# Kernel optimization log

Hardware: AMD Instinct MI355X
Metric: run time of the kernel (lower is better)

The kernel has to match this reference:

```python
import jax, jax.numpy as jnp
import numpy as np

N = 12000   # nodes (multiple of 120)
E = 192000  # edges
T = 120     # utterances per dialogue
IN = 192
OUT = 6


def _edge_softmax(logits, dst, n):
    # logits: [E, H] -> softmax over incoming edges of each dst node
    m = jax.ops.segment_max(logits, dst, num_segments=n)
    ex = jnp.exp(logits - m[dst])
    s = jax.ops.segment_sum(ex, dst, num_segments=n)
    return ex / s[dst]


def _gatv2(h, src, dst, Wsrc, bsrc, Wdst, bdst, attn, Wres, n):
    # DGL GATv2Conv: e = attn . leakyrelu(fc_src(h)[u] + fc_dst(h)[v]), residual, relu activation
    Hh, F = attn.shape
    fs = (h @ Wsrc + bsrc).reshape(n, Hh, F)
    fd = (h @ Wdst + bdst).reshape(n, Hh, F)
    e = jax.nn.leaky_relu(fs[src] + fd[dst], 0.2)          # [E, H, F]
    logits = jnp.einsum('ehf,hf->eh', e, attn)              # [E, H]
    alpha = _edge_softmax(logits, dst, n)                   # [E, H]
    out = jax.ops.segment_sum(alpha[:, :, None] * fs[src], dst, num_segments=n)
    res = (h @ Wres).reshape(n, Hh, F)
    return jax.nn.relu(out + res)                           # [N, H, F]


def _lstm_dir(x, Wih, Whh, bih, bhh, reverse):
    # x: [T, B, D]; torch gate order i, f, g, o
    B = x.shape[1]
    hid = Whh.shape[1]
    def step(carry, xt):
        h, c = carry
        z = xt @ Wih.T + h @ Whh.T + bih + bhh
        i, f, g, o = jnp.split(z, 4, axis=-1)
        c = jax.nn.sigmoid(f) * c + jax.nn.sigmoid(i) * jnp.tanh(g)
        h = jax.nn.sigmoid(o) * jnp.tanh(c)
        return (h, c), h
    init = (jnp.zeros((B, hid), x.dtype), jnp.zeros((B, hid), x.dtype))
    _, hs = jax.lax.scan(step, init, x, reverse=reverse)
    return hs


def setup_inputs() -> dict:
    key = jax.random.key(0)
    ks = iter(jax.random.split(key, 64))
    def rn(shape, s=0.05):
        return jax.random.normal(next(ks), shape, jnp.float32) * s
    inp = {
        'text': rn((N, 1024), 1.0),
        'audio': rn((N, 512), 1.0),
        'vision': rn((N, 1024), 1.0),
        'edge_src': jax.random.randint(next(ks), (E,), 0, N, jnp.int32),
        'edge_dst': jax.random.randint(next(ks), (E,), 0, N, jnp.int32),
        # modality encoders
        'W_audio': rn((512, 64)), 'b_audio': jnp.zeros((64,), jnp.float32),
        'W_vision': rn((1024, 64)), 'b_vision': jnp.zeros((64,), jnp.float32),
        'W_text': rn((1024, 64)), 'b_text': jnp.zeros((64,), jnp.float32),
        # bidirectional LSTM (hidden=4 -> 16 gate rows)
        'Wih_f': rn((16, IN)), 'Whh_f': rn((16, 4)), 'bih_f': jnp.zeros((16,), jnp.float32), 'bhh_f': jnp.zeros((16,), jnp.float32),
        'Wih_b': rn((16, IN)), 'Whh_b': rn((16, 4)), 'bih_b': jnp.zeros((16,), jnp.float32), 'bhh_b': jnp.zeros((16,), jnp.float32),
        # imputation GraphConv (192->192, norm='both')
        'W_gc': rn((IN, IN)), 'b_gc': jnp.zeros((IN,), jnp.float32),
        # gat2 (cross-modal multi-head GAT, 192 -> 16 heads x 4)
        'Wsrc2': rn((IN, 64)), 'bsrc2': jnp.zeros((64,), jnp.float32),
        'Wdst2': rn((IN, 64)), 'bdst2': jnp.zeros((64,), jnp.float32),
        'attn2': rn((16, 4)), 'Wres2': rn((IN, 64)),
        # gat1 layer 0 (192 -> 16 heads x 32)
        'Wsrc0': rn((IN, 512)), 'bsrc0': jnp.zeros((512,), jnp.float32),
        'Wdst0': rn((IN, 512)), 'bdst0': jnp.zeros((512,), jnp.float32),
        'attn0': rn((16, 32)), 'Wres0': rn((IN, 512)),
        # gat1 layer 1 (512 -> 16 heads x 4)
        'Wsrc1': rn((512, 64)), 'bsrc1': jnp.zeros((64,), jnp.float32),
        'Wdst1': rn((512, 64)), 'bdst1': jnp.zeros((64,), jnp.float32),
        'attn1': rn((16, 4)), 'Wres1': rn((512, 64)),
        # final classifier Linear(136, out_size)
        'W_lin': rn((136, OUT)), 'b_lin': jnp.zeros((OUT,), jnp.float32),
    }
    return inp


def reference(text, audio, vision, edge_src, edge_dst,
              W_audio, b_audio, W_vision, b_vision, W_text, b_text,
              Wih_f, Whh_f, bih_f, bhh_f, Wih_b, Whh_b, bih_b, bhh_b,
              W_gc, b_gc,
              Wsrc2, bsrc2, Wdst2, bdst2, attn2, Wres2,
              Wsrc0, bsrc0, Wdst0, bdst0, attn0, Wres0,
              Wsrc1, bsrc1, Wdst1, bdst1, attn1, Wres1,
              W_lin, b_lin):
    n = text.shape[0]
    # modality encoders (dropout is identity at inference)
    t = text @ W_text + b_text
    a = audio @ W_audio + b_audio
    v = vision @ W_vision + b_vision
    stackFT = jnp.concatenate([t, a, v], axis=1)            # [N, 192]

    # bidirectional LSTM over dialogues of length T=120
    x = stackFT.reshape(-1, T, IN).transpose(1, 0, 2)       # [T, B, 192]
    hf = _lstm_dir(x, Wih_f, Whh_f, bih_f, bhh_f, False)
    hb = _lstm_dir(x, Wih_b, Whh_b, bih_b, bhh_b, True)
    newFeature = jnp.concatenate([hf, hb], -1).transpose(1, 0, 2).reshape(n, 8)

    # GraphConv imputation, norm='both' (degrees clamped to 1 as in DGL)
    ones = jnp.ones((edge_src.shape[0],), stackFT.dtype)
    deg_out = jnp.maximum(jax.ops.segment_sum(ones, edge_src, num_segments=n), 1.0)
    deg_in = jnp.maximum(jax.ops.segment_sum(ones, edge_dst, num_segments=n), 1.0)
    hw = (stackFT @ W_gc) * (deg_out ** -0.5)[:, None]
    h1 = jax.ops.segment_sum(hw[edge_src], edge_dst, num_segments=n) * (deg_in ** -0.5)[:, None] + b_gc
    h = 0.5 * (stackFT + h1)
    # F.normalize(h, p=1)
    h = h / jnp.maximum(jnp.sum(jnp.abs(h), axis=1, keepdims=True), 1e-12)

    # cross-modal multi-head GAT branch -> [N, 64]
    h3 = _gatv2(h, edge_src, edge_dst, Wsrc2, bsrc2, Wdst2, bdst2, attn2, Wres2, n).reshape(n, -1)

    # stacked GATv2 layers
    h = _gatv2(h, edge_src, edge_dst, Wsrc0, bsrc0, Wdst0, bdst0, attn0, Wres0, n).reshape(n, -1)  # [N, 512]
    h = _gatv2(h, edge_src, edge_dst, Wsrc1, bsrc1, Wdst1, bdst1, attn1, Wres1, n).reshape(n, -1)  # [N, 64]

    out = jnp.concatenate([h, newFeature, h3], axis=1) @ W_lin + b_lin  # [N, out_size]
    return out
```

## Files before the change

### kernel.cpp

```cpp
#include <hip/hip_runtime.h>

typedef __attribute__((ext_vector_type(8))) short short8;
typedef __attribute__((ext_vector_type(4))) float f32x4;
typedef _Float16 half8v __attribute__((ext_vector_type(8)));
typedef _Float16 half4v __attribute__((ext_vector_type(4)));

__device__ __forceinline__ unsigned short f2bf(float f) {
    unsigned u = __float_as_uint(f);
    u += 0x7FFFu + ((u >> 16) & 1u);
    return (unsigned short)(u >> 16);
}
__device__ __forceinline__ float bf2f(unsigned short h) {
    return __uint_as_float((unsigned)h << 16);
}

template<int MF, int OUTMODE>
__global__ __launch_bounds__(256)
void gemm_v7(const unsigned short* __restrict__ A, const unsigned short* __restrict__ B,
             const float* __restrict__ bias, const float* __restrict__ rowscale,
             void* __restrict__ Cv, const float* __restrict__ fin_num,
             const float* __restrict__ fin_den,
             int M, int Nb, int K, int ldc)
{
    __shared__ alignas(16) unsigned short As[MF * 64 * 32];
    __shared__ alignas(16) unsigned short Bs[4 * 64 * 8];
    const int t = threadIdx.x;
    const int w = t >> 6, l = t & 63;
    const int r16 = l & 15, kg = l >> 4;
    const int row0 = blockIdx.x * (64 * MF);
    const int col0 = blockIdx.y * 64;
    const int bcol = t & 63, bkg = t >> 6;

    f32x4 acc[MF][4] = {};
    const short8 z8 = {0, 0, 0, 0, 0, 0, 0, 0};

    int srow[MF], sch[MF];
    bool va[MF];
    const unsigned short* aptr[MF];
#pragma unroll
    for (int it = 0; it < MF; ++it) {
        int idx = it * 256 + t;
        srow[it] = idx >> 2; sch[it] = idx & 3;
        int gm = row0 + srow[it];
        va[it] = gm < M;
        aptr[it] = A + (size_t)gm * K + sch[it] * 8;
    }
    const unsigned short* bptr = B + (size_t)(bkg * 8) * Nb + col0 + bcol;

    short8 pa[MF];
    unsigned short pbv[8];
#pragma unroll
    for (int it = 0; it < MF; ++it)
        pa[it] = va[it] ? *reinterpret_cast<const short8*>(aptr[it]) : z8;
#pragma unroll
    for (int j = 0; j < 8; ++j) pbv[j] = bptr[(size_t)j * Nb];

    for (int k0 = 0; k0 < K; k0 += 32) {
#pragma unroll
        for (int it = 0; it < MF; ++it)
            *reinterpret_cast<short8*>(&As[srow[it] * 32 + sch[it] * 8]) = pa[it];
        {
            short8 hv;
#pragma unroll
            for (int j = 0; j < 8; ++j) hv[j] = (short)pbv[j];
            *reinterpret_cast<short8*>(&Bs[bkg * 512 + bcol * 8]) = hv;
        }
        __syncthreads();
        if (k0 + 32 < K) {
#pragma unroll
            for (int it = 0; it < MF; ++it)
                pa[it] = va[it] ? *reinterpret_cast<const short8*>(aptr[it] + k0 + 32) : z8;
#pragma unroll
            for (int j = 0; j < 8; ++j) pbv[j] = bptr[(size_t)(k0 + 32 + j) * Nb];
        }
        short8 af[MF];
#pragma unroll
        for (int mi = 0; mi < MF; ++mi)
            af[mi] = *reinterpret_cast<const short8*>(&As[((w * MF + mi) * 16 + r16) * 32 + kg * 8]);
#pragma unroll
        for (int ni = 0; ni < 4; ++ni) {
            short8 bf = *reinterpret_cast<const short8*>(&Bs[kg * 512 + (ni * 16 + r16) * 8]);
#pragma unroll
            for (int mi = 0; mi < MF; ++mi)
                acc[mi][ni] = __builtin_amdgcn_mfma_f32_16x16x32_bf16(af[mi], bf, acc[mi][ni], 0, 0, 0);
        }
        __syncthreads();
    }
#pragma unroll
    for (int mi = 0; mi < MF; ++mi)
#pragma unroll
        for (int ni = 0; ni < 4; ++ni) {
            int col = col0 + ni * 16 + r16;
            float bv = bias ? bias[col] : 0.f;
#pragma unroll
            for (int r = 0; r < 4; ++r) {
                int gm = row0 + (w * MF + mi) * 16 + kg * 4 + r;
                if (gm < M) {
                    float val = acc[mi][ni][r] + bv;
                    if (rowscale) val *= rowscale[gm];
                    size_t idx = (size_t)gm * ldc + col;
                    if (OUTMODE == 0) {
                        ((float*)Cv)[idx] = val;
                    } else if (OUTMODE == 1) {
                        ((unsigned short*)Cv)[idx] = f2bf(val);
                    } else {
                        float d = fin_den[(size_t)gm * 16 + (col >> 5)];
                        float inv = (d > 0.f) ? __fdividef(1.f, d) : 0.f;
                        float o = fmaxf(fin_num[idx] * inv + val, 0.f);
                        ((unsigned short*)Cv)[idx] = f2bf(o);
                    }
                }
            }
        }
}

__global__ __launch_bounds__(256)
void enc_f16(const float* __restrict__ text, const float* __restrict__ audio, const float* __restrict__ vision,
             const _Float16* __restrict__ Wf16,
             const float* __restrict__ bt, const float* __restrict__ ba, const float* __restrict__ bv,
             float* __restrict__ Cf, unsigned short* __restrict__ Cb, int M)
{
    __shared__ alignas(16) _Float16 Af[32 * 32];
    __shared__ alignas(16) _Float16 Bf[4 * 64 * 8];
    const int z = blockIdx.z;
    const float* A  = (z == 0) ? text : (z == 1) ? audio : vision;
    const _Float16* W = Wf16 + ((z == 0) ? 0 : (z == 1) ? 65536 : 98304);
    const float* bb = (z == 0) ? bt : (z == 1) ? ba : bv;
    const int K = (z == 1) ? 512 : 1024;

    const int t = threadIdx.x;
    const int w = t >> 6, l = t & 63;
    const int r16 = l & 15, kg = l >> 4;
    const int row0 = blockIdx.x * 32;
    const int mi = w & 1;
    const int ncol0 = (w >> 1) * 32;
    const int arow = t >> 3, ac8 = t & 7;
    const int bcol = t & 63, bkg = t >> 6;

    const float* ap = A + (size_t)(row0 + arow) * K + ac8 * 4;
    const _Float16* wp = W + (size_t)(bkg * 8) * 64 + bcol;

    float4 pa = *reinterpret_cast<const float4*>(ap);
    _Float16 pb[8];
#pragma unroll
    for (int j = 0; j < 8; ++j) pb[j] = wp[(size_t)j * 64];

    f32x4 acc[2] = {};
    for (int k0 = 0; k0 < K; k0 += 32) {
        {
            half4v av;
            av[0] = (_Float16)pa.x; av[1] = (_Float16)pa.y;
            av[2] = (_Float16)pa.z; av[3] = (_Float16)pa.w;
            *reinterpret_cast<half4v*>(&Af[arow * 32 + ac8 * 4]) = av;
            half8v bv8;
#pragma unroll
            for (int j = 0; j < 8; ++j) bv8[j] = pb[j];
            *reinterpret_cast<half8v*>(&Bf[bkg * 512 + bcol * 8]) = bv8;
        }
        __syncthreads();
        if (k0 + 32 < K) {
            pa = *reinterpret_cast<const float4*>(ap + k0 + 32);
#pragma unroll
            for (int j = 0; j < 8; ++j) pb[j] = wp[(size_t)(k0 + 32 + j) * 64];
        }
        half8v af = *reinterpret_cast<const half8v*>(&Af[(mi * 16 + r16) * 32 + kg * 8]);
#pragma unroll
        for (int ni = 0; ni < 2; ++ni) {
            half8v bf = *reinterpret_cast<const half8v*>(&Bf[kg * 512 + (ncol0 + ni * 16 + r16) * 8]);
            acc[ni] = __builtin_amdgcn_mfma_f32_16x16x32_f16(af, bf, acc[ni], 0, 0, 0);
        }
        __syncthreads();
    }
#pragma unroll
    for (int ni = 0; ni < 2; ++ni) {
        int col = ncol0 + ni * 16 + r16;
        float bvv = bb[col];
#pragma unroll
        for (int r = 0; r < 4; ++r) {
            int gr = row0 + mi * 16 + kg * 4 + r;
            if (gr < M) {
                float val = acc[ni][r] + bvv;
                size_t idx = (size_t)gr * 192 + z * 64 + col;
                Cf[idx] = val;
                Cb[idx] = f2bf(val);
            }
        }
    }
}

__global__ void pack3b(const float* __restrict__ W0, const float* __restrict__ W1, const float* __restrict__ W2,
                       const float* __restrict__ b0, const float* __restrict__ b1,
                       unsigned short* __restrict__ Wp, float* __restrict__ bp, int K, int O)
{
    int gid = blockIdx.x * blockDim.x + threadIdx.x;
    int O3 = 3 * O;
    if (gid < O3) bp[gid] = (gid < O) ? b0[gid] : (gid < 2 * O) ? b1[gid - O] : 0.f;
    if (gid >= K * O3) return;
    int k = gid / O3, c = gid - k * O3;
    float v = (c < O) ? W0[k * O + c] : (c < 2 * O) ? W1[k * O + c - O] : W2[k * O + c - 2 * O];
    Wp[gid] = f2bf(v);
}

__global__ void pack2b(const float* __restrict__ W0, const float* __restrict__ W1,
                       const float* __restrict__ b0, const float* __restrict__ b1,
                       unsigned short* __restrict__ Wp, float* __restrict__ bp, int K, int O)
{
    int gid = blockIdx.x * blockDim.x + threadIdx.x;
    int O2 = 2 * O;
    if (gid < O2) bp[gid] = (gid < O) ? b0[gid] : b1[gid - O];
    if (gid >= K * O2) return;
    int k = gid / O2, c = gid - k * O2;
    Wp[gid] = f2bf((c < O) ? W0[k * O + c] : W1[k * O + c - O]);
}

__global__ void pack1b(const float* __restrict__ W, unsigned short* __restrict__ Wp, int cnt)
{
    int gid = blockIdx.x * blockDim.x + threadIdx.x;
    if (gid < cnt) Wp[gid] = f2bf(W[gid]);
}

__global__ void pack_encw(const float* __restrict__ Wt, const float* __restrict__ Wa, const float* __restrict__ Wv,
                          _Float16* __restrict__ out)
{
    int gid = blockIdx.x * blockDim.x + threadIdx.x;
    if (gid >= 163840) return;
    float v;
    if (gid < 65536) v = Wt[gid];
    else if (gid < 98304) v = Wa[gid - 65536];
    else v = Wv[gid - 98304];
    out[gid] = (_Float16)v;
}

__global__ void deg_kernel(const int* __restrict__ src, const int* __restrict__ dst,
                           int* degout, int* degin, int E)
{
    int e = blockIdx.x * blockDim.x + threadIdx.x;
    if (e < E) {
        atomicAdd(&degout[src[e]], 1);
        atomicAdd(&degin[dst[e]], 1);
    }
}

__global__ __launch_bounds__(1024)
void scan_kernel(const int* __restrict__ degin, int* __restrict__ rowstart, int n)
{
    __shared__ int part[1024];
    int t = threadIdx.x;
    int chunk = (n + 1023) / 1024;
    int s = 0;
    for (int i = 0; i < chunk; ++i) {
        int idx = t * chunk + i;
        if (idx < n) s += degin[idx];
    }
    part[t] = s;
    __syncthreads();
    for (int o = 1; o < 1024; o <<= 1) {
        int v = (t >= o) ? part[t - o] : 0;
        __syncthreads();
        part[t] += v;
        __syncthreads();
    }
    int run = (t > 0) ? part[t - 1] : 0;
    for (int i = 0; i < chunk; ++i) {
        int idx = t * chunk + i;
        if (idx < n) { rowstart[idx] = run; run += degin[idx]; }
    }
    if (t == 1023) rowstart[n] = part[1023];
}

__global__ void perm_kernel(const int* __restrict__ dst, const int* __restrict__ rowstart,
                            int* cursor, int* __restrict__ perm, int E)
{
    int e = blockIdx.x * blockDim.x + threadIdx.x;
    if (e < E) {
        int v = dst[e];
        int p = atomicAdd(&cursor[v], 1);
        perm[rowstart[v] + p] = e;
    }
}

__global__ void gather_src_kernel(const int* __restrict__ esrc, int* perm, int E)
{
    int i = blockIdx.x * blockDim.x + threadIdx.x;
    if (i < E) perm[i] = esrc[perm[i]];
}

__global__ void rs_kernel(const int* degout, const int* degin, float* rso, float* rsi, int n)
{
    int i = blockIdx.x * blockDim.x + threadIdx.x;
    if (i < n) {
        rso[i] = rsqrtf((float)max(degout[i], 1));
        rsi[i] = rsqrtf((float)max(degin[i], 1));
    }
}

__global__ void lstm_pre(const float* __restrict__ x, const float* __restrict__ Wf,
                         const float* __restrict__ Wb,
                         const float* bf1, const float* bf2, const float* bb1, const float* bb2,
                         float* __restrict__ xWf, float* __restrict__ xWb, int n)
{
    int gid = blockIdx.x * blockDim.x + threadIdx.x;
    if (gid >= n * 32) return;
    int nn = gid >> 5, r = gid & 31, d = r >> 4, j = r & 15;
    const float* W = (d ? Wb : Wf) + j * 192;
    const float* xr = x + (size_t)nn * 192;
    float s = 0.f;
#pragma unroll 4
    for (int k = 0; k < 192; k += 4) {
        float4 xv = *reinterpret_cast<const float4*>(xr + k);
        float4 wv = *reinterpret_cast<const float4*>(W + k);
        s += xv.x * wv.x + xv.y * wv.y + xv.z * wv.z + xv.w * wv.w;
    }
    s += d ? (bb1[j] + bb2[j]) : (bf1[j] + bf2[j]);
    int b = nn / 120, tt = nn - b * 120;
    (d ? xWb : xWf)[((size_t)b * 16 + j) * 120 + tt] = s;
}

__device__ __forceinline__ float fsigm(float x) { return __fdividef(1.f, 1.f + __expf(-x)); }
__device__ __forceinline__ float ftanh(float x) { return 1.f - __fdividef(2.f, __expf(2.f * x) + 1.f); }

template<int DIR>
__device__ void lstm_chain(const float* __restrict__ xw, const float* __restrict__ whh,
                           float* __restrict__ newF, int b)
{
    int j = threadIdx.x & 15;
    int k = j & 3;
    float4 w = *reinterpret_cast<const float4*>(whh + j * 4);
    const float* xp = xw + ((size_t)b * 16 + j) * 120;
    float h0 = 0.f, h1 = 0.f, h2 = 0.f, h3 = 0.f, cst = 0.f;
    int tb0 = DIR ? 108 : 0;
    float4 a0 = *reinterpret_cast<const float4*>(xp + tb0);
    float4 a1 = *reinterpret_cast<const float4*>(xp + tb0 + 4);
    float4 a2 = *reinterpret_cast<const float4*>(xp + tb0 + 8);
    for (int ch = 0; ch < 10; ++ch) {
        float4 b0 = a0, b1 = a1, b2 = a2;
        if (ch < 9) {
            int nt = DIR ? (96 - ch * 12) : (12 + ch * 12);
            b0 = *reinterpret_cast<const float4*>(xp + nt);
            b1 = *reinterpret_cast<const float4*>(xp + nt + 4);
            b2 = *reinterpret_cast<const float4*>(xp + nt + 8);
        }
        float zz[12] = {a0.x, a0.y, a0.z, a0.w, a1.x, a1.y, a1.z, a1.w, a2.x, a2.y, a2.z, a2.w};
        int tbase = DIR ? (108 - ch * 12) : (ch * 12);
#pragma unroll
        for (int ii = 0; ii < 12; ++ii) {
            int idx = DIR ? (11 - ii) : ii;
            float z = zz[idx] + ((w.x * h0 + w.y * h1) + (w.z * h2 + w.w * h3));
            float zi = __shfl(z, k, 16);
            float zf = __shfl(z, k + 4, 16);
            float zg = __shfl(z, k + 8, 16);
            float zo = __shfl(z, k + 12, 16);
            float ig = fsigm(zi), fg = fsigm(zf), gg = ftanh(zg), og = fsigm(zo);
            cst = fg * cst + ig * gg;
            float hn = og * ftanh(cst);
            h0 = __shfl(hn, 0, 16); h1 = __shfl(hn, 1, 16);
            h2 = __shfl(hn, 2, 16); h3 = __shfl(hn, 3, 16);
            if (j < 4) newF[((size_t)b * 120 + tbase + idx) * 8 + DIR * 4 + j] = hn;
        }
        a0 = b0; a1 = b1; a2 = b2;
    }
}

__global__ __launch_bounds__(64)
void lstm_seq2(const float* __restrict__ xWf, const float* __restrict__ xWb,
               const float* __restrict__ Whhf, const float* __restrict__ Whhb,
               float* __restrict__ newF, int B)
{
    int sub = threadIdx.x >> 4;
    int chain = blockIdx.x * 4 + sub;
    if (chain >= 2 * B) return;
    int d = chain / B;
    int b = chain - d * B;
    if (d == 0) lstm_chain<0>(xWf, Whhf, newF, b);
    else        lstm_chain<1>(xWb, Whhb, newF, b);
}

__global__ __launch_bounds__(256)
void gc_combine5(const float* __restrict__ stackFT, const unsigned short* __restrict__ hw,
                 const int* __restrict__ rowstart, const int* __restrict__ csrc,
                 const float* __restrict__ rs_in,
                 const float* __restrict__ b_gc, unsigned short* __restrict__ hB, int n)
{
    int v = blockIdx.x * 4 + (threadIdx.x >> 6);
    int l = threadIdx.x & 63;
    if (v >= n) return;
    int s0 = rowstart[v], s1 = rowstart[v + 1];
    float sum0 = 0.f, sum1 = 0.f, sum2 = 0.f;

    unsigned short a0 = 0, a1 = 0, a2 = 0, b0 = 0, b1 = 0, b2 = 0;
    auto LD = [&](int i, unsigned short& x0, unsigned short& x1, unsigned short& x2) {
        const unsigned short* hr = hw + (size_t)csrc[i] * 192 + l;
        x0 = hr[0]; x1 = hr[64]; x2 = hr[128];
    };
    int i = s0;
    if (i < s1) LD(i, a0, a1, a2);
    if (i + 1 < s1) LD(i + 1, b0, b1, b2);
    for (; i + 2 < s1; i += 2) {
        unsigned short n0, n1, n2, m0 = 0, m1 = 0, m2 = 0;
        LD(i + 2, n0, n1, n2);
        if (i + 3 < s1) LD(i + 3, m0, m1, m2);
        sum0 += bf2f(a0) + bf2f(b0);
        sum1 += bf2f(a1) + bf2f(b1);
        sum2 += bf2f(a2) + bf2f(b2);
        a0 = n0; a1 = n1; a2 = n2; b0 = m0; b1 = m1; b2 = m2;
    }
    if (i < s1) { sum0 += bf2f(a0); sum1 += bf2f(a1); sum2 += bf2f(a2); }
    if (i + 1 < s1) { sum0 += bf2f(b0); sum1 += bf2f(b1); sum2 += bf2f(b2); }

    float ri = rs_in[v];
    const float* sf = stackFT + (size_t)v * 192 + l;
    float v0 = 0.5f * (sf[0]   + sum0 * ri + b_gc[l]);
    float v1 = 0.5f * (sf[64]  + sum1 * ri + b_gc[l + 64]);
    float v2 = 0.5f * (sf[128] + sum2 * ri + b_gc[l + 128]);
    float r = fabsf(v0) + fabsf(v1) + fabsf(v2);
#pragma unroll
    for (int o = 32; o; o >>= 1) r += __shfl_xor(r, o);
    float inv = __fdividef(1.f, fmaxf(r, 1e-12f));
    unsigned short* hp = hB + (size_t)v * 192 + l;
    hp[0]   = f2bf(v0 * inv);
    hp[64]  = f2bf(v1 * inv);
    hp[128] = f2bf(v2 * inv);
}

__global__ __launch_bounds__(256)
void gat_edge4c(const unsigned short* __restrict__ base,
                const float* __restrict__ attn,
                const int* __restrict__ rowstart, const int* __restrict__ csrc,
                float* __restrict__ outp, int n)
{
    int v = blockIdx.x * 16 + (threadIdx.x >> 4);
    int l = threadIdx.x & 15;
    if (v >= n) return;
    float4 at = *reinterpret_cast<const float4*>(attn + l * 4);
    ushort4 fdu = *reinterpret_cast<const ushort4*>(base + (size_t)v * 192 + 64 + l * 4);
    float fd0 = bf2f(fdu.x), fd1 = bf2f(fdu.y), fd2 = bf2f(fdu.z), fd3 = bf2f(fdu.w);
    float ac0 = 0.f, ac1 = 0.f, ac2 = 0.f, ac3 = 0.f, dn = 0.f;
    int s0 = rowstart[v], s1 = rowstart[v + 1];

    auto LD = [&](int i) -> ushort4 {
        return *reinterpret_cast<const ushort4*>(base + (size_t)csrc[i] * 192 + l * 4);
    };
    auto ACC = [&](ushort4 su) {
        float s0f = bf2f(su.x), s1f = bf2f(su.y), s2f = bf2f(su.z), s3f = bf2f(su.w);
        float e0 = s0f + fd0; e0 = fmaxf(e0, 0.2f * e0);
        float e1 = s1f + fd1; e1 = fmaxf(e1, 0.2f * e1);
        float e2 = s2f + fd2; e2 = fmaxf(e2, 0.2f * e2);
        float e3 = s3f + fd3; e3 = fmaxf(e3, 0.2f * e3);
        float p = e0 * at.x + e1 * at.y + e2 * at.z + e3 * at.w;
        float ex = __expf(p);
        ac0 += ex * s0f; ac1 += ex * s1f; ac2 += ex * s2f; ac3 += ex * s3f;
        dn += ex;
    };
    const ushort4 zu = make_ushort4(0, 0, 0, 0);
    ushort4 c0 = zu, c1 = zu;
    int i = s0;
    if (i < s1) c0 = LD(i);
    if (i + 1 < s1) c1 = LD(i + 1);
    for (; i + 2 < s1; i += 2) {
        ushort4 n0 = LD(i + 2);
        ushort4 n1 = (i + 3 < s1) ? LD(i + 3) : zu;
        ACC(c0); ACC(c1);
        c0 = n0; c1 = n1;
    }
    if (i < s1) ACC(c0);
    if (i + 1 < s1) ACC(c1);

    ushort4 ru = *reinterpret_cast<const ushort4*>(base + (size_t)v * 192 + 128 + l * 4);
    float inv = (dn > 0.f) ? __fdividef(1.f, dn) : 0.f;
    float4 o;
    o.x = fmaxf(ac0 * inv + bf2f(ru.x), 0.f);
    o.y = fmaxf(ac1 * inv + bf2f(ru.y), 0.f);
    o.z = fmaxf(ac2 * inv + bf2f(ru.z), 0.f);
    o.w = fmaxf(ac3 * inv + bf2f(ru.w), 0.f);
    *reinterpret_cast<float4*>(outp + (size_t)v * 64 + l * 4) = o;
}

__global__ __launch_bounds__(256)
void gat_edge32b(const unsigned short* __restrict__ base,
                 const float* __restrict__ attn,
                 const int* __restrict__ rowstart, const int* __restrict__ csrc,
                 float* __restrict__ num, float* __restrict__ den, int n)
{
    int v = blockIdx.x * 4 + (threadIdx.x >> 6);
    int l = threadIdx.x & 63;
    if (v >= n) return;
    float at[8];
    {
        float4 aA = *reinterpret_cast<const float4*>(attn + l * 8);
        float4 aB = *reinterpret_cast<const float4*>(attn + l * 8 + 4);
        at[0] = aA.x; at[1] = aA.y; at[2] = aA.z; at[3] = aA.w;
        at[4] = aB.x; at[5] = aB.y; at[6] = aB.z; at[7] = aB.w;
    }
    float fd[8];
    {
        short8 fdu = *reinterpret_cast<const short8*>(base + (size_t)v * 1024 + 512 + l * 8);
#pragma unroll
        for (int j = 0; j < 8; ++j) fd[j] = bf2f((unsigned short)fdu[j]);
    }
    float acc[8] = {};
    float dn = 0.f;
    int s0 = rowstart[v], s1 = rowstart[v + 1];

    auto LD = [&](int i) -> short8 {
        return *reinterpret_cast<const short8*>(base + (size_t)csrc[i] * 1024 + l * 8);
    };
    auto ACC = [&](short8 su) {
        float sf[8];
        float p = 0.f;
#pragma unroll
        for (int j = 0; j < 8; ++j) {
            sf[j] = bf2f((unsigned short)su[j]);
            float e = sf[j] + fd[j];
            e = fmaxf(e, 0.2f * e);
            p += e * at[j];
        }
        p += __shfl_xor(p, 1, 4);
        p += __shfl_xor(p, 2, 4);
        float ex = __expf(p);
#pragma unroll
        for (int j = 0; j < 8; ++j) acc[j] += ex * sf[j];
        dn += ex;
    };
    const short8 z8 = {0, 0, 0, 0, 0, 0, 0, 0};
    short8 c0 = z8, c1 = z8;
    int i = s0;
    if (i < s1) c0 = LD(i);
    if (i + 1 < s1) c1 = LD(i + 1);
    for (; i + 2 < s1; i += 2) {
        short8 n0 = LD(i + 2);
        short8 n1 = (i + 3 < s1) ? LD(i + 3) : z8;
        ACC(c0); ACC(c1);
        c0 = n0; c1 = n1;
    }
    if (i < s1) ACC(c0);
    if (i + 1 < s1) ACC(c1);

    float* np = num + (size_t)v * 512 + l * 8;
    *reinterpret_cast<float4*>(np)     = make_float4(acc[0], acc[1], acc[2], acc[3]);
    *reinterpret_cast<float4*>(np + 4) = make_float4(acc[4], acc[5], acc[6], acc[7]);
    if ((l & 3) == 0) den[(size_t)v * 16 + (l >> 2)] = dn;
}

__global__ void final_lin(const float* __restrict__ h1, const float* __restrict__ newF,
                          const float* __restrict__ h3, const float* __restrict__ W,
                          const float* __restrict__ bias, float* __restrict__ out, int n)
{
    int gid = blockIdx.x * blockDim.x + threadIdx.x;
    if (gid >= n * 6) return;
    int v = gid / 6, o = gid - v * 6;
    float s = bias[o];
    const float* a = h1 + (size_t)v * 64;
#pragma unroll 8
    for (int r = 0; r < 64; ++r) s += a[r] * W[r * 6 + o];
    const float* b = newF + (size_t)v * 8;
#pragma unroll
    for (int r = 0; r < 8; ++r) s += b[r] * W[(64 + r) * 6 + o];
    const float* c = h3 + (size_t)v * 64;
#pragma unroll 8
    for (int r = 0; r < 64; ++r) s += c[r] * W[(72 + r) * 6 + o];
    out[gid] = s;
}

extern "C" void kernel_launch(void* const* d_in, const int* in_sizes, int n_in,
                              void* d_out, int out_size, void* d_ws, size_t ws_size,
                              hipStream_t stream)
{
    const float* text   = (const float*)d_in[0];
    const float* audio  = (const float*)d_in[1];
    const float* vision = (const float*)d_in[2];
    const int*   esrc   = (const int*)d_in[3];
    const int*   edst   = (const int*)d_in[4];
    const float* W_audio = (const float*)d_in[5];  const float* b_audio = (const float*)d_in[6];
    const float* W_vision= (const float*)d_in[7];  const float* b_vision= (const float*)d_in[8];
    const float* W_text  = (const float*)d_in[9];  const float* b_text  = (const float*)d_in[10];
    const float* Wih_f = (const float*)d_in[11]; const float* Whh_f = (const float*)d_in[12];
    const float* bih_f = (const float*)d_in[13]; const float* bhh_f = (const float*)d_in[14];
    const float* Wih_b = (const float*)d_in[15]; const float* Whh_b = (const float*)d_in[16];
    const float* bih_b = (const float*)d_in[17]; const float* bhh_b = (const float*)d_in[18];
    const float* W_gc  = (const float*)d_in[19]; const float* b_gc  = (const float*)d_in[20];
    const float* Wsrc2 = (const float*)d_in[21]; const float* bsrc2 = (const float*)d_in[22];
    const float* Wdst2 = (const float*)d_in[23]; const float* bdst2 = (const float*)d_in[24];
    const float* attn2 = (const float*)d_in[25]; const float* Wres2 = (const float*)d_in[26];
    const float* Wsrc0 = (const float*)d_in[27]; const float* bsrc0 = (const float*)d_in[28];
    const float* Wdst0 = (const float*)d_in[29]; const float* bdst0 = (const float*)d_in[30];
    const float* attn0 = (const float*)d_in[31]; const float* Wres0 = (const float*)d_in[32];
    const float* Wsrc1 = (const float*)d_in[33]; const float* bsrc1 = (const float*)d_in[34];
    const float* Wdst1 = (const float*)d_in[35]; const float* bdst1 = (const float*)d_in[36];
    const float* attn1 = (const float*)d_in[37]; const float* Wres1 = (const float*)d_in[38];
    const float* W_lin = (const float*)d_in[39]; const float* b_lin = (const float*)d_in[40];
    float* out = (float*)d_out;

    const int n = in_sizes[0] / 1024;
    const int E = in_sizes[3];
    const int B = n / 120;

    char* p = (char*)d_ws;
    auto alloc_f = [&](size_t cnt) { float* r = (float*)p; p += ((cnt * 4 + 255) / 256) * 256; return r; };
    auto alloc_h = [&](size_t cnt) { unsigned short* r = (unsigned short*)p; p += ((cnt * 2 + 255) / 256) * 256; return r; };
    auto alloc_i = [&](size_t cnt) { int* r = (int*)p; p += ((cnt * 4 + 255) / 256) * 256; return r; };
    float*          stackFT = alloc_f((size_t)n * 192);
    unsigned short* stackBF = alloc_h((size_t)n * 192);
    unsigned short* hbufBF  = alloc_h((size_t)n * 192);
    unsigned short* encW    = alloc_h(163840);
    float* xWf     = alloc_f((size_t)n * 16);
    float* xWb     = alloc_f((size_t)n * 16);
    float* newF    = alloc_f((size_t)n * 8);
    float* big0    = alloc_f((size_t)n * 512);
    float* big1    = alloc_f((size_t)n * 512);
    float* big2    = alloc_f((size_t)n * 512);
    float* den     = alloc_f((size_t)n * 16);
    float* h3      = alloc_f((size_t)n * 64);
    float* h1s     = alloc_f((size_t)n * 64);
    float* rs_out  = alloc_f(n);
    float* rs_in   = alloc_f(n);
    int* zero_base = alloc_i((size_t)3 * n);
    int* degout = zero_base;
    int* degin  = zero_base + n;
    int* cursor = zero_base + 2 * n;
    int* rowstart = alloc_i((size_t)n + 1);
    int* perm     = alloc_i((size_t)E);
    if ((size_t)(p - (char*)d_ws) > ws_size) return;

    unsigned short* pw = (unsigned short*)h1s;
    float* pb = h1s + 120000;

    hipMemsetAsync(zero_base, 0, (size_t)3 * n * 4, stream);
    deg_kernel<<<(E + 255) / 256, 256, 0, stream>>>(esrc, edst, degout, degin, E);
    scan_kernel<<<1, 1024, 0, stream>>>(degin, rowstart, n);
    perm_kernel<<<(E + 255) / 256, 256, 0, stream>>>(edst, rowstart, cursor, perm, E);
    gather_src_kernel<<<(E + 255) / 256, 256, 0, stream>>>(esrc, perm, E);
    rs_kernel<<<(n + 255) / 256, 256, 0, stream>>>(degout, degin, rs_out, rs_in, n);
    const int* csrc = perm;

    auto gemm = [&](auto mf_tag, auto om_tag, const unsigned short* A, const unsigned short* Bm,
                    const float* bias, const float* rsc, void* Cp,
                    const float* fnum, const float* fden, int M, int Nb, int K, int ldc) {
        constexpr int MF = decltype(mf_tag)::value;
        constexpr int OM = decltype(om_tag)::value;
        dim3 grid((M + 64 * MF - 1) / (64 * MF), Nb / 64);
        gemm_v7<MF, OM><<<grid, 256, 0, stream>>>(A, Bm, bias, rsc, Cp, fnum, fden, M, Nb, K, ldc);
    };
    using I1 = std::integral_constant<int, 1>;
    using I2 = std::integral_constant<int, 2>;
    using O1 = std::integral_constant<int, 1>;
    using O2 = std::integral_constant<int, 2>;

    pack_encw<<<(163840 + 255) / 256, 256, 0, stream>>>(W_text, W_audio, W_vision, (_Float16*)encW);
    {
        dim3 grid(n / 32, 1, 3);
        enc_f16<<<grid, 256, 0, stream>>>(text, audio, vision, (const _Float16*)encW,
                                          b_text, b_audio, b_vision, stackFT, stackBF, n);
    }

    lstm_pre<<<(n * 32 + 255) / 256, 256, 0, stream>>>(stackFT, Wih_f, Wih_b,
                                                       bih_f, bhh_f, bih_b, bhh_b, xWf, xWb, n);
    lstm_seq2<<<(2 * B + 3) / 4, 64, 0, stream>>>(xWf, xWb, Whh_f, Whh_b, newF, B);

    pack1b<<<(192 * 192 + 255) / 256, 256, 0, stream>>>(W_gc, pw, 192 * 192);
    gemm(I1{}, O1{}, stackBF, pw, nullptr, rs_out, big0, nullptr, nullptr, n, 192, 192, 192);
    gc_combine5<<<(n + 3) / 4, 256, 0, stream>>>(stackFT, (const unsigned short*)big0,
                                                 rowstart, csrc, rs_in, b_gc, hbufBF, n);

    pack3b<<<(192 * 192 + 255) / 256, 256, 0, stream>>>(Wsrc2, Wdst2, Wres2, bsrc2, bdst2, pw, pb, 192, 64);
    gemm(I1{}, O1{}, hbufBF, pw, pb, nullptr, big0, nullptr, nullptr, n, 192, 192, 192);
    gat_edge4c<<<(n + 15) / 16, 256, 0, stream>>>((const unsigned short*)big0, attn2, rowstart, csrc, h3, n);

    pack2b<<<(192 * 1024 + 255) / 256, 256, 0, stream>>>(Wsrc0, Wdst0, bsrc0, bdst0, pw, pb, 192, 512);
    gemm(I2{}, O1{}, hbufBF, pw, pb, nullptr, big0, nullptr, nullptr, n, 1024, 192, 1024);
    gat_edge32b<<<(n + 3) / 4, 256, 0, stream>>>((const unsigned short*)big0, attn0, rowstart, csrc, big2, den, n);
    pack1b<<<(192 * 512 + 255) / 256, 256, 0, stream>>>(Wres0, pw, 192 * 512);
    gemm(I1{}, O2{}, hbufBF, pw, nullptr, nullptr, big1, big2, den, n, 512, 192, 512);

    pack3b<<<(512 * 192 + 255) / 256, 256, 0, stream>>>(Wsrc1, Wdst1, Wres1, bsrc1, bdst1, pw, pb, 512, 64);
    gemm(I1{}, O1{}, (const unsigned short*)big1, pw, pb, nullptr, big0, nullptr, nullptr, n, 192, 512, 192);
    gat_edge4c<<<(n + 15) / 16, 256, 0, stream>>>((const unsigned short*)big0, attn1, rowstart, csrc, h1s, n);

    final_lin<<<(n * 6 + 255) / 256, 256, 0, stream>>>(h1s, newF, h3, W_lin, b_lin, out, n);
}
```

Measured before the change: 350.3 us.

## Merge weight packing into one kernel and double encoder K-step with swizzled LDS

Six separate weight pack launches (encoder fp16 plus five bf16 GEMM weight packs) become one pack_all kernel. Each GEMM now reads its weights from a fixed offset in a shared buffer, which removes per-stage launch gaps. The encoder GEMM now loads 64 K-elements per iteration, using 8-wide A loads and an XOR-swizzled A tile in shared memory. This halves the loop trips and barriers and should reduce LDS bank conflicts. The packed weights are now stored in the h1s buffer, so they must not overlap it before the final gat_edge4c overwrites h1s.

```diff
diff --git a/kernel.cpp b/kernel.cpp
--- a/kernel.cpp
+++ b/kernel.cpp
@@ -3,7 +3,6 @@
 typedef __attribute__((ext_vector_type(8))) short short8;
 typedef __attribute__((ext_vector_type(4))) float f32x4;
 typedef _Float16 half8v __attribute__((ext_vector_type(8)));
-typedef _Float16 half4v __attribute__((ext_vector_type(4)));
 
 __device__ __forceinline__ unsigned short f2bf(float f) {
     unsigned u = __float_as_uint(f);
@@ -115,13 +114,13 @@
 }
 
 __global__ __launch_bounds__(256)
-void enc_f16(const float* __restrict__ text, const float* __restrict__ audio, const float* __restrict__ vision,
-             const _Float16* __restrict__ Wf16,
-             const float* __restrict__ bt, const float* __restrict__ ba, const float* __restrict__ bv,
-             float* __restrict__ Cf, unsigned short* __restrict__ Cb, int M)
-{
-    __shared__ alignas(16) _Float16 Af[32 * 32];
-    __shared__ alignas(16) _Float16 Bf[4 * 64 * 8];
+void enc_f16v2(const float* __restrict__ text, const float* __restrict__ audio, const float* __restrict__ vision,
+               const _Float16* __restrict__ Wf16,
+               const float* __restrict__ bt, const float* __restrict__ ba, const float* __restrict__ bv,
+               float* __restrict__ Cf, unsigned short* __restrict__ Cb, int M)
+{
+    __shared__ alignas(16) _Float16 Af[32 * 64];
+    __shared__ alignas(16) _Float16 Bf[8 * 64 * 8];
     const int z = blockIdx.z;
     const float* A  = (z == 0) ? text : (z == 1) ? audio : vision;
     const _Float16* W = Wf16 + ((z == 0) ? 0 : (z == 1) ? 65536 : 98304);
@@ -135,39 +134,50 @@
     const int mi = w & 1;
     const int ncol0 = (w >> 1) * 32;
     const int arow = t >> 3, ac8 = t & 7;
-    const int bcol = t & 63, bkg = t >> 6;
-
-    const float* ap = A + (size_t)(row0 + arow) * K + ac8 * 4;
-    const _Float16* wp = W + (size_t)(bkg * 8) * 64 + bcol;
-
-    float4 pa = *reinterpret_cast<const float4*>(ap);
-    _Float16 pb[8];
-#pragma unroll
-    for (int j = 0; j < 8; ++j) pb[j] = wp[(size_t)j * 64];
+    const int bcol = t & 63, bw = t >> 6;
+
+    const float* ap = A + (size_t)(row0 + arow) * K + ac8 * 8;
+    const _Float16* wp = W + (size_t)(bw * 16) * 64 + bcol;
+
+    float4 pa0 = *reinterpret_cast<const float4*>(ap);
+    float4 pa1 = *reinterpret_cast<const float4*>(ap + 4);
+    _Float16 pb[16];
+#pragma unroll
+    for (int j = 0; j < 16; ++j) pb[j] = wp[(size_t)j * 64];
 
     f32x4 acc[2] = {};
-    for (int k0 = 0; k0 < K; k0 += 32) {
+    const int asw = ac8 ^ (arow & 7);
+    for (int k0 = 0; k0 < K; k0 += 64) {
         {
-            half4v av;
-            av[0] = (_Float16)pa.x; av[1] = (_Float16)pa.y;
-            av[2] = (_Float16)pa.z; av[3] = (_Float16)pa.w;
-            *reinterpret_cast<half4v*>(&Af[arow * 32 + ac8 * 4]) = av;
-            half8v bv8;
-#pragma unroll
-            for (int j = 0; j < 8; ++j) bv8[j] = pb[j];
-            *reinterpret_cast<half8v*>(&Bf[bkg * 512 + bcol * 8]) = bv8;
+            half8v av;
+            av[0] = (_Float16)pa0.x; av[1] = (_Float16)pa0.y;
+            av[2] = (_Float16)pa0.z; av[3] = (_Float16)pa0.w;
+            av[4] = (_Float16)pa1.x; av[5] = (_Float16)pa1.y;
+            av[6] = (_Float16)pa1.z; av[7] = (_Float16)pa1.w;
+            *reinterpret_cast<half8v*>(&Af[arow * 64 + asw * 8]) = av;
+            half8v b0, b1;
+#pragma unroll
+            for (int j = 0; j < 8; ++j) { b0[j] = pb[j]; b1[j] = pb[8 + j]; }
+            *reinterpret_cast<half8v*>(&Bf[(bw * 2) * 512 + bcol * 8]) = b0;
+            *reinterpret_cast<half8v*>(&Bf[(bw * 2 + 1) * 512 + bcol * 8]) = b1;
         }
         __syncthreads();
-        if (k0 + 32 < K) {
-            pa = *reinterpret_cast<const float4*>(ap + k0 + 32);
-#pragma unroll
-            for (int j = 0; j < 8; ++j) pb[j] = wp[(size_t)(k0 + 32 + j) * 64];
-        }
-        half8v af = *reinterpret_cast<const half8v*>(&Af[(mi * 16 + r16) * 32 + kg * 8]);
+        if (k0 + 64 < K) {
+            pa0 = *reinterpret_cast<const float4*>(ap + k0 + 64);
+            pa1 = *reinterpret_cast<const float4*>(ap + k0 + 68);
+#pragma unroll
+            for (int j = 0; j < 16; ++j) pb[j] = wp[(size_t)(k0 + 64 + j) * 64];
+        }
+        const int row = mi * 16 + r16;
+        half8v afA = *reinterpret_cast<const half8v*>(&Af[row * 64 + (kg ^ (row & 7)) * 8]);
+        half8v afB = *reinterpret_cast<const half8v*>(&Af[row * 64 + ((kg + 4) ^ (row & 7)) * 8]);
 #pragma unroll
         for (int ni = 0; ni < 2; ++ni) {
-            half8v bf = *reinterpret_cast<const half8v*>(&Bf[kg * 512 + (ncol0 + ni * 16 + r16) * 8]);
-            acc[ni] = __builtin_amdgcn_mfma_f32_16x16x32_f16(af, bf, acc[ni], 0, 0, 0);
+            int cx = (ncol0 + ni * 16 + r16) * 8;
+            half8v bf0 = *reinterpret_cast<const half8v*>(&Bf[kg * 512 + cx]);
+            half8v bf1 = *reinterpret_cast<const half8v*>(&Bf[(kg + 4) * 512 + cx]);
+            acc[ni] = __builtin_amdgcn_mfma_f32_16x16x32_f16(afA, bf0, acc[ni], 0, 0, 0);
+            acc[ni] = __builtin_amdgcn_mfma_f32_16x16x32_f16(afB, bf1, acc[ni], 0, 0, 0);
         }
         __syncthreads();
     }
@@ -188,47 +198,46 @@
     }
 }
 
-__global__ void pack3b(const float* __restrict__ W0, const float* __restrict__ W1, const float* __restrict__ W2,
-                       const float* __restrict__ b0, const float* __restrict__ b1,
-                       unsigned short* __restrict__ Wp, float* __restrict__ bp, int K, int O)
+__global__ void pack_all(const float* __restrict__ Wt, const float* __restrict__ Wa, const float* __restrict__ Wv,
+                         const float* __restrict__ Wgc,
+                         const float* __restrict__ Ws2, const float* __restrict__ Wd2, const float* __restrict__ Wr2,
+                         const float* __restrict__ bs2, const float* __restrict__ bd2,
+                         const float* __restrict__ Ws0, const float* __restrict__ Wd0,
+                         const float* __restrict__ bs0, const float* __restrict__ bd0,
+                         const float* __restrict__ Wr0,
+                         const float* __restrict__ Ws1, const float* __restrict__ Wd1, const float* __restrict__ Wr1,
+                         const float* __restrict__ bs1, const float* __restrict__ bd1,
+                         _Float16* __restrict__ encW, unsigned short* __restrict__ Wall, float* __restrict__ ball)
 {
     int gid = blockIdx.x * blockDim.x + threadIdx.x;
-    int O3 = 3 * O;
-    if (gid < O3) bp[gid] = (gid < O) ? b0[gid] : (gid < 2 * O) ? b1[gid - O] : 0.f;
-    if (gid >= K * O3) return;
-    int k = gid / O3, c = gid - k * O3;
-    float v = (c < O) ? W0[k * O + c] : (c < 2 * O) ? W1[k * O + c - O] : W2[k * O + c - 2 * O];
-    Wp[gid] = f2bf(v);
-}
-
-__global__ void pack2b(const float* __restrict__ W0, const float* __restrict__ W1,
-                       const float* __restrict__ b0, const float* __restrict__ b1,
-                       unsigned short* __restrict__ Wp, float* __restrict__ bp, int K, int O)
-{
-    int gid = blockIdx.x * blockDim.x + threadIdx.x;
-    int O2 = 2 * O;
-    if (gid < O2) bp[gid] = (gid < O) ? b0[gid] : b1[gid - O];
-    if (gid >= K * O2) return;
-    int k = gid / O2, c = gid - k * O2;
-    Wp[gid] = f2bf((c < O) ? W0[k * O + c] : W1[k * O + c - O]);
-}
-
-__global__ void pack1b(const float* __restrict__ W, unsigned short* __restrict__ Wp, int cnt)
-{
-    int gid = blockIdx.x * blockDim.x + threadIdx.x;
-    if (gid < cnt) Wp[gid] = f2bf(W[gid]);
-}
-
-__global__ void pack_encw(const float* __restrict__ Wt, const float* __restrict__ Wa, const float* __restrict__ Wv,
-                          _Float16* __restrict__ out)
-{
-    int gid = blockIdx.x * blockDim.x + threadIdx.x;
-    if (gid >= 163840) return;
-    float v;
-    if (gid < 65536) v = Wt[gid];
-    else if (gid < 98304) v = Wa[gid - 65536];
-    else v = Wv[gid - 98304];
-    out[gid] = (_Float16)v;
+    if (gid < 163840) {
+        float v = (gid < 65536) ? Wt[gid] : (gid < 98304) ? Wa[gid - 65536] : Wv[gid - 98304];
+        encW[gid] = (_Float16)v;
+    }
+    if (gid < 36864) {
+        Wall[gid] = f2bf(Wgc[gid]);
+    } else if (gid < 73728) {
+        int i = gid - 36864, k = i / 192, c = i - k * 192;
+        float v = (c < 64) ? Ws2[k * 64 + c] : (c < 128) ? Wd2[k * 64 + c - 64] : Wr2[k * 64 + c - 128];
+        Wall[gid] = f2bf(v);
+    } else if (gid < 270336) {
+        int i = gid - 73728, k = i >> 10, c = i & 1023;
+        float v = (c < 512) ? Ws0[k * 512 + c] : Wd0[k * 512 + c - 512];
+        Wall[gid] = f2bf(v);
+    } else if (gid < 368640) {
+        Wall[gid] = f2bf(Wr0[gid - 270336]);
+    } else if (gid < 466944) {
+        int i = gid - 368640, k = i / 192, c = i - k * 192;
+        float v = (c < 64) ? Ws1[k * 64 + c] : (c < 128) ? Wd1[k * 64 + c - 64] : Wr1[k * 64 + c - 128];
+        Wall[gid] = f2bf(v);
+    } else if (gid < 468352) {
+        int i = gid - 466944;
+        float v;
+        if (i < 192)       v = (i < 64) ? bs2[i] : (i < 128) ? bd2[i - 64] : 0.f;
+        else if (i < 1216) { int j = i - 192; v = (j < 512) ? bs0[j] : bd0[j - 512]; }
+        else               { int j = i - 1216; v = (j < 64) ? bs1[j] : (j < 128) ? bd1[j - 64] : 0.f; }
+        ball[i] = v;
+    }
 }
 
 __global__ void deg_kernel(const int* __restrict__ src, const int* __restrict__ dst,
@@ -621,10 +630,24 @@
     int* perm     = alloc_i((size_t)E);
     if ((size_t)(p - (char*)d_ws) > ws_size) return;
 
-    unsigned short* pw = (unsigned short*)h1s;
-    float* pb = h1s + 120000;
+    unsigned short* Wall = (unsigned short*)h1s;
+    float* ball = h1s + 240000;
+    const unsigned short* Wp_gc = Wall;
+    const unsigned short* Wp_g2 = Wall + 36864;
+    const unsigned short* Wp_g0 = Wall + 73728;
+    const unsigned short* Wp_r0 = Wall + 270336;
+    const unsigned short* Wp_g1 = Wall + 368640;
+    const float* bp_g2 = ball;
+    const float* bp_g0 = ball + 192;
+    const float* bp_g1 = ball + 1216;
 
     hipMemsetAsync(zero_base, 0, (size_t)3 * n * 4, stream);
+    pack_all<<<(468352 + 255) / 256, 256, 0, stream>>>(
+        W_text, W_audio, W_vision, W_gc,
+        Wsrc2, Wdst2, Wres2, bsrc2, bdst2,
+        Wsrc0, Wdst0, bsrc0, bdst0, Wres0,
+        Wsrc1, Wdst1, Wres1, bsrc1, bdst1,
+        (_Float16*)encW, Wall, ball);
     deg_kernel<<<(E + 255) / 256, 256, 0, stream>>>(esrc, edst, degout, degin, E);
     scan_kernel<<<1, 1024, 0, stream>>>(degin, rowstart, n);
     perm_kernel<<<(E + 255) / 256, 256, 0, stream>>>(edst, rowstart, cursor, perm, E);
@@ -645,34 +668,28 @@
     using O1 = std::integral_constant<int, 1>;
     using O2 = std::integral_constant<int, 2>;
 
-    pack_encw<<<(163840 + 255) / 256, 256, 0, stream>>>(W_text, W_audio, W_vision, (_Float16*)encW);
     {
         dim3 grid(n / 32, 1, 3);
-        enc_f16<<<grid, 256, 0, stream>>>(text, audio, vision, (const _Float16*)encW,
-                                          b_text, b_audio, b_vision, stackFT, stackBF, n);
+        enc_f16v2<<<grid, 256, 0, stream>>>(text, audio, vision, (const _Float16*)encW,
+                                            b_text, b_audio, b_vision, stackFT, stackBF, n);
     }
 
     lstm_pre<<<(n * 32 + 255) / 256, 256, 0, stream>>>(stackFT, Wih_f, Wih_b,
                                                        bih_f, bhh_f, bih_b, bhh_b, xWf, xWb, n);
     lstm_seq2<<<(2 * B + 3) / 4, 64, 0, stream>>>(xWf, xWb, Whh_f, Whh_b, newF, B);
 
-    pack1b<<<(192 * 192 + 255) / 256, 256, 0, stream>>>(W_gc, pw, 192 * 192);
-    gemm(I1{}, O1{}, stackBF, pw, nullptr, rs_out, big0, nullptr, nullptr, n, 192, 192, 192);
+    gemm(I1{}, O1{}, stackBF, Wp_gc, nullptr, rs_out, big0, nullptr, nullptr, n, 192, 192, 192);
     gc_combine5<<<(n + 3) / 4, 256, 0, stream>>>(stackFT, (const unsigned short*)big0,
                                                  rowstart, csrc, rs_in, b_gc, hbufBF, n);
 
-    pack3b<<<(192 * 192 + 255) / 256, 256, 0, stream>>>(Wsrc2, Wdst2, Wres2, bsrc2, bdst2, pw, pb, 192, 64);
-    gemm(I1{}, O1{}, hbufBF, pw, pb, nullptr, big0, nullptr, nullptr, n, 192, 192, 192);
+    gemm(I1{}, O1{}, hbufBF, Wp_g2, bp_g2, nullptr, big0, nullptr, nullptr, n, 192, 192, 192);
     gat_edge4c<<<(n + 15) / 16, 256, 0, stream>>>((const unsigned short*)big0, attn2, rowstart, csrc, h3, n);
 
-    pack2b<<<(192 * 1024 + 255) / 256, 256, 0, stream>>>(Wsrc0, Wdst0, bsrc0, bdst0, pw, pb, 192, 512);
-    gemm(I2{}, O1{}, hbufBF, pw, pb, nullptr, big0, nullptr, nullptr, n, 1024, 192, 1024);
+    gemm(I2{}, O1{}, hbufBF, Wp_g0, bp_g0, nullptr, big0, nullptr, nullptr, n, 1024, 192, 1024);
     gat_edge32b<<<(n + 3) / 4, 256, 0, stream>>>((const unsigned short*)big0, attn0, rowstart, csrc, big2, den, n);
-    pack1b<<<(192 * 512 + 255) / 256, 256, 0, stream>>>(Wres0, pw, 192 * 512);
-    gemm(I1{}, O2{}, hbufBF, pw, nullptr, nullptr, big1, big2, den, n, 512, 192, 512);
-
-    pack3b<<<(512 * 192 + 255) / 256, 256, 0, stream>>>(Wsrc1, Wdst1, Wres1, bsrc1, bdst1, pw, pb, 512, 64);
-    gemm(I1{}, O1{}, (const unsigned short*)big1, pw, pb, nullptr, big0, nullptr, nullptr, n, 192, 512, 192);
+    gemm(I1{}, O2{}, hbufBF, Wp_r0, nullptr, nullptr, big1, big2, den, n, 512, 192, 512);
+
+    gemm(I1{}, O1{}, (const unsigned short*)big1, Wp_g1, bp_g1, nullptr, big0, nullptr, nullptr, n, 192, 512, 192);
     gat_edge4c<<<(n + 15) / 16, 256, 0, stream>>>((const unsigned short*)big0, attn1, rowstart, csrc, h1s, n);
 
     final_lin<<<(n * 6 + 255) / 256, 256, 0, stream>>>(h1s, newF, h3, W_lin, b_lin, out, n);
```

New measurement: 344.2 us. No clear change (-1.7%).
